# Optimization experiments

Hardware: AMD Instinct MI355X
Metric: run time of the kernel (lower is better)

The kernel has to match this reference:

```python
import jax, jax.numpy as jnp
import numpy as np

K_CONST = 1.0  # margin constant K from __init__


def setup_inputs() -> dict:
    key = jax.random.key(0)
    k1, k2, k3 = jax.random.split(key, 3)
    m, n, d = 2048, 100000, 128
    return {
        "X_tilde": jax.random.normal(k1, (m, d), dtype=jnp.float32),
        "X": jax.random.normal(k2, (n, d), dtype=jnp.float32),
        "w": jax.random.normal(k3, (n, 1), dtype=jnp.float32),
        "k": 10,
    }


def reference(X_tilde, X, w, k):
    # w_prime = sqrt((max(w) - w) / K), appended as extra coordinate for the
    # augmented exact L2 search (queries padded with 0 in that coordinate).
    w_prime2 = (jnp.max(w) - w)[:, 0] / K_CONST  # (n,) == w_prime**2
    # squared L2 in augmented space: ||q||^2 + ||x||^2 + w_prime^2 - 2 q.x
    q2 = jnp.sum(X_tilde * X_tilde, axis=1, keepdims=True)           # (m,1)
    x2 = jnp.sum(X * X, axis=1) + w_prime2                            # (n,)
    d2 = q2 + x2[None, :] - 2.0 * (X_tilde @ X.T)                     # (m,n)
    _, idx = jax.lax.top_k(-d2, k)                                    # (m,k) nearest
    # gather neighbors and recompute actual (non-augmented) L2 distance
    nb = X[idx]                                                       # (m,k,d)
    diff = nb - X_tilde[:, None, :]
    dist = jnp.sqrt(jnp.sum(diff * diff, axis=2))                     # (m,k)
    act = w[idx, 0] - K_CONST * dist                                  # (m,k)
    # argmax + gather == max over the k neighbors
    return jnp.max(act, axis=1)                                       # (m,)
```

## Files before the change

kernel.cpp:

```cpp
#include <hip/hip_runtime.h>
#include <math.h>

typedef __attribute__((ext_vector_type(8))) short short8;
typedef __attribute__((ext_vector_type(16))) float f32x16;

#define D      128
#define NSEG   128
#define SEGC   800
#define NT     25
#define TILE_C 32
#define KTOP   10
#define CAP    128
#define DELTA  3.0f
#define NPAD   (NSEG * SEGC + TILE_C)
#define ROWU   144
#define TUNITS (TILE_C * 18)
#define BUFU   (TUNITS * 8)

__device__ __forceinline__ int lds_unit(int u) {
    int r = u / 18, kb = u % 18;
    return r * 18 + (kb ^ ((r >> 2) & 1));
}

__device__ __forceinline__ ushort f2bf(float f) {
    uint u = __float_as_uint(f);
    uint r = (u + 0x7FFFu + ((u >> 16) & 1u)) >> 16;
    return (ushort)r;
}

__device__ __forceinline__ uint packx2(float x2w) {
    ushort h = f2bf(x2w);
    float hf = __uint_as_float(((uint)h) << 16);
    ushort lo = f2bf(x2w - hf);
    return (uint)h | ((uint)lo << 16);
}

__device__ __forceinline__ void insert10(float s, float v, float ls[KTOP], float lw[KTOP]) {
    ls[9] = s; lw[9] = v;
#pragma unroll
    for (int p = 9; p > 0; --p) {
        bool sw = ls[p] < ls[p - 1];
        float ts = sw ? ls[p - 1] : ls[p];
        float tl = sw ? ls[p]     : ls[p - 1];
        float tv = sw ? lw[p - 1] : lw[p];
        float tu = sw ? lw[p]     : lw[p - 1];
        ls[p] = ts; ls[p - 1] = tl;
        lw[p] = tv; lw[p - 1] = tu;
    }
}

__device__ __forceinline__ void insert10s(float s, float ms[KTOP]) {
    ms[9] = s;
#pragma unroll
    for (int p = 9; p > 0; --p) {
        float a = fminf(ms[p - 1], ms[p]);
        float b = fmaxf(ms[p - 1], ms[p]);
        ms[p - 1] = a; ms[p] = b;
    }
}

__global__ void prep_kernel(const float* __restrict__ Xt, const float* __restrict__ X,
                            const float* __restrict__ w,
                            ushort* __restrict__ Xbp, ushort* __restrict__ Xtb,
                            float* __restrict__ x2wf, float* __restrict__ q2f,
                            int* __restrict__ cnt, int n, int m, int nblocksA) {
    int wave = threadIdx.x >> 6, lane = threadIdx.x & 63;
    if ((int)blockIdx.x < nblocksA) {
        int row = blockIdx.x * 4 + wave;
        if (row >= NPAD) return;
        ushort* rowp = Xbp + (size_t)row * ROWU;
        if (row < n) {
            float2 v = ((const float2*)X)[(size_t)row * 64 + lane];
            ((ushort2*)rowp)[lane] = make_ushort2(f2bf(v.x), f2bf(v.y));
            float s = v.x * v.x + v.y * v.y;
#pragma unroll
            for (int o = 32; o; o >>= 1) s += __shfl_xor(s, o, 64);
            float x2w = s - w[row];
            if (lane == 0) x2wf[row] = x2w;
            if (lane < 8) ((uint*)rowp)[64 + lane] = (lane == 0) ? packx2(x2w) : 0u;
        } else {
            ((ushort2*)rowp)[lane] = make_ushort2(0, 0);
            if (lane < 8) ((uint*)rowp)[64 + lane] = (lane == 0) ? packx2(1e30f) : 0u;
        }
    } else {
        int qb = blockIdx.x - nblocksA;
        int row = qb * 4 + wave;
        int tid = qb * 256 + threadIdx.x;
        if (tid < m) cnt[tid] = 0;
        if (row >= m) return;
        float2 v = ((const float2*)Xt)[(size_t)row * 64 + lane];
        ((ushort2*)Xtb)[(size_t)row * 64 + lane] = make_ushort2(f2bf(v.x), f2bf(v.y));
        float s = v.x * v.x + v.y * v.y;
#pragma unroll
        for (int o = 32; o; o >>= 1) s += __shfl_xor(s, o, 64);
        if (lane == 0) q2f[row] = s;
    }
}

__device__ __forceinline__ void emit_cand(int q, int c, int* cnt, int* buf) {
    int pos = atomicAdd(&cnt[q], 1);
    if (pos < CAP) buf[q * CAP + pos] = c;
}

template<int PASS>
__global__ __launch_bounds__(256, 2) void nd_pass(
        const ushort* __restrict__ Xbp, const ushort* __restrict__ Xtb,
        const float* __restrict__ tau, float* __restrict__ minbuf,
        int* __restrict__ cnt, int* __restrict__ buf, int m) {
    __shared__ __align__(16) ushort As[2 * BUFU];

    const int t = threadIdx.x;
    const int l = t & 63, wv = t >> 6;
    const int half = l >> 5;
    const int seg = blockIdx.x;
    const int qbase = blockIdx.y * 512 + wv * 128;
    const int q0 = qbase + (l & 31);
    const int tile0 = seg * NT;
    const int halfx = half ^ ((l >> 2) & 1);

    short8 Bf[9][4];
#pragma unroll
    for (int s = 0; s < 8; ++s)
#pragma unroll
        for (int qs = 0; qs < 4; ++qs)
            Bf[s][qs] = *(const short8*)(Xtb + (size_t)(q0 + qs * 32) * D + s * 16 + half * 8);
    {
        short8 z = (short8)(short)0;
        if (l < 32) { z[0] = (short)0xBF00; z[1] = (short)0xBF00; }
#pragma unroll
        for (int qs = 0; qs < 4; ++qs) Bf[8][qs] = z;
    }

    float tp[4];
    float mx[4];
#pragma unroll
    for (int qs = 0; qs < 4; ++qs) {
        tp[qs] = (PASS == 2) ? (-0.5f * tau[q0 + qs * 32]) : 0.f;
        mx[qs] = -INFINITY;
    }

    const int u0 = t, u1 = 256 + t, u2 = 512 + (t & 63);
    const int L0 = lds_unit(u0) * 8, L1 = lds_unit(u1) * 8, L2 = lds_unit(u2) * 8;
    const uint4* Xg = (const uint4*)Xbp;

    uint4 r0 = Xg[(size_t)tile0 * TUNITS + u0];
    uint4 r1 = Xg[(size_t)tile0 * TUNITS + u1];
    uint4 r2 = make_uint4(0, 0, 0, 0);
    if (t < 64) r2 = Xg[(size_t)tile0 * TUNITS + u2];

    for (int t2 = 0; t2 < NT; ++t2) {
        ushort* Lb = &As[(t2 & 1) * BUFU];
        *(uint4*)&Lb[L0] = r0;
        *(uint4*)&Lb[L1] = r1;
        if (t < 64) *(uint4*)&Lb[L2] = r2;
        __syncthreads();

        const size_t gb = (size_t)(tile0 + t2 + 1) * TUNITS;
        r0 = Xg[gb + u0];
        r1 = Xg[gb + u1];
        if (t < 64) r2 = Xg[gb + u2];

        f32x16 acc0 = (f32x16)0.f, acc1 = (f32x16)0.f, acc2 = (f32x16)0.f, acc3 = (f32x16)0.f;
#pragma unroll
        for (int ks = 0; ks < 9; ++ks) {
            const int kb = (ks < 8) ? (ks * 2 + halfx) : (16 + halfx);
            short8 a = *(const short8*)&Lb[((l & 31) * 18 + kb) * 8];
            acc0 = __builtin_amdgcn_mfma_f32_32x32x16_bf16(a, Bf[ks][0], acc0, 0, 0, 0);
            acc1 = __builtin_amdgcn_mfma_f32_32x32x16_bf16(a, Bf[ks][1], acc1, 0, 0, 0);
            acc2 = __builtin_amdgcn_mfma_f32_32x32x16_bf16(a, Bf[ks][2], acc2, 0, 0, 0);
            acc3 = __builtin_amdgcn_mfma_f32_32x32x16_bf16(a, Bf[ks][3], acc3, 0, 0, 0);
        }

        float h[4];
#pragma unroll
        for (int qs = 0; qs < 4; ++qs) h[qs] = -INFINITY;
#pragma unroll
        for (int r = 0; r < 16; ++r) {
            h[0] = fmaxf(h[0], acc0[r]); h[1] = fmaxf(h[1], acc1[r]);
            h[2] = fmaxf(h[2], acc2[r]); h[3] = fmaxf(h[3], acc3[r]);
        }
        if (PASS == 1) {
#pragma unroll
            for (int qs = 0; qs < 4; ++qs) mx[qs] = fmaxf(mx[qs], h[qs]);
        } else {
            const int base = (tile0 + t2) * TILE_C;
            if (__any(h[0] >= tp[0])) {
#pragma unroll
                for (int r = 0; r < 16; ++r)
                    if (acc0[r] >= tp[0]) emit_cand(q0,      base + (r & 3) + 8 * (r >> 2) + 4 * half, cnt, buf);
            }
            if (__any(h[1] >= tp[1])) {
#pragma unroll
                for (int r = 0; r < 16; ++r)
                    if (acc1[r] >= tp[1]) emit_cand(q0 + 32, base + (r & 3) + 8 * (r >> 2) + 4 * half, cnt, buf);
            }
            if (__any(h[2] >= tp[2])) {
#pragma unroll
                for (int r = 0; r < 16; ++r)
                    if (acc2[r] >= tp[2]) emit_cand(q0 + 64, base + (r & 3) + 8 * (r >> 2) + 4 * half, cnt, buf);
            }
            if (__any(h[3] >= tp[3])) {
#pragma unroll
                for (int r = 0; r < 16; ++r)
                    if (acc3[r] >= tp[3]) emit_cand(q0 + 96, base + (r & 3) + 8 * (r >> 2) + 4 * half, cnt, buf);
            }
        }
    }

    if (PASS == 1) {
        size_t rowi = (size_t)(seg * 2 + half) * m;
#pragma unroll
        for (int qs = 0; qs < 4; ++qs)
            minbuf[rowi + q0 + qs * 32] = -2.f * mx[qs];
    }
}

__global__ void tau_kernel(const float* __restrict__ minbuf, float* __restrict__ tau, int m) {
    __shared__ float sh[64 * 40];
    const int qi = threadIdx.x & 63, part = threadIdx.x >> 6;
    const int q = blockIdx.x * 64 + qi;
    float ms[KTOP];
#pragma unroll
    for (int e = 0; e < KTOP; ++e) ms[e] = INFINITY;
#pragma unroll 4
    for (int i = 0; i < 64; ++i) {
        float v = minbuf[(size_t)(part * 64 + i) * m + q];
        if (v < ms[9]) insert10s(v, ms);
    }
#pragma unroll
    for (int e = 0; e < KTOP; ++e) sh[qi * 40 + part * 10 + e] = ms[e];
    __syncthreads();
    if (threadIdx.x < 64) {
        const int qq = blockIdx.x * 64 + threadIdx.x;
        float fs[KTOP];
#pragma unroll
        for (int e = 0; e < KTOP; ++e) fs[e] = INFINITY;
        for (int x = 0; x < 40; ++x) {
            float v = sh[threadIdx.x * 40 + x];
            if (v < fs[9]) insert10s(v, fs);
        }
        tau[qq] = fs[9] + DELTA;
    }
}

__global__ void rescore_kernel(const float* __restrict__ Xtf, const float* __restrict__ Xf,
                               const float* __restrict__ w, const float* __restrict__ x2wf,
                               const float* __restrict__ q2f, const int* __restrict__ cnt,
                               const int* __restrict__ buf, float* __restrict__ out, int m) {
    __shared__ float sS[CAP], sW[CAP];
    const int q = blockIdx.x, l = threadIdx.x;
    const int c = min(cnt[q], CAP);
    const bool v0 = l < c, v1 = l + 64 < c;
    const int j0 = v0 ? buf[q * CAP + l] : 0;
    const int j1 = v1 ? buf[q * CAP + l + 64] : 0;
    const float4* Q4 = (const float4*)Xtf + (size_t)q * 32;
    const float4* A4 = (const float4*)Xf + (size_t)j0 * 32;
    const float4* B4 = (const float4*)Xf + (size_t)j1 * 32;
    float acc0 = 0.f, acc1 = 0.f;
#pragma unroll 8
    for (int d = 0; d < 32; ++d) {
        float4 qv = Q4[d];
        float4 a = A4[d], b = B4[d];
        acc0 = fmaf(qv.x, a.x, fmaf(qv.y, a.y, fmaf(qv.z, a.z, fmaf(qv.w, a.w, acc0))));
        acc1 = fmaf(qv.x, b.x, fmaf(qv.y, b.y, fmaf(qv.z, b.z, fmaf(qv.w, b.w, acc1))));
    }
    sS[l]      = v0 ? (x2wf[j0] - 2.f * acc0) : INFINITY;
    sW[l]      = v0 ? w[j0] : 0.f;
    sS[l + 64] = v1 ? (x2wf[j1] - 2.f * acc1) : INFINITY;
    sW[l + 64] = v1 ? w[j1] : 0.f;
    __syncthreads();
    if (l == 0) {
        float ls[KTOP], lw[KTOP];
#pragma unroll
        for (int e = 0; e < KTOP; ++e) { ls[e] = INFINITY; lw[e] = 0.f; }
        for (int i = 0; i < c; ++i)
            if (sS[i] < ls[9]) insert10(sS[i], sW[i], ls, lw);
        float q2v = q2f[q];
        float mxv = -INFINITY;
#pragma unroll
        for (int e = 0; e < KTOP; ++e) {
            if (ls[e] < 1e30f) {
                float d2 = fmaxf(q2v + ls[e] + lw[e], 0.f);
                mxv = fmaxf(mxv, lw[e] - sqrtf(d2));
            }
        }
        out[q] = mxv;
    }
}

extern "C" void kernel_launch(void* const* d_in, const int* in_sizes, int n_in,
                              void* d_out, int out_size, void* d_ws, size_t ws_size,
                              hipStream_t stream) {
    const float* Xt = (const float*)d_in[0];
    const float* X  = (const float*)d_in[1];
    const float* w  = (const float*)d_in[2];
    const int m = in_sizes[0] / D;
    const int n = in_sizes[1] / D;

    auto align256 = [](size_t x) { return (x + 255) & ~(size_t)255; };
    char* p = (char*)d_ws;
    ushort* Xbp  = (ushort*)p;  p += align256((size_t)NPAD * ROWU * 2);
    ushort* Xtb  = (ushort*)p;  p += align256((size_t)m * D * 2);
    float*  x2wf = (float*)p;   p += align256((size_t)n * 4);
    float*  q2f  = (float*)p;   p += align256((size_t)m * 4);
    float*  minb = (float*)p;   p += align256((size_t)2 * NSEG * m * 4);
    float*  tau  = (float*)p;   p += align256((size_t)m * 4);
    int*    cnt  = (int*)p;     p += align256((size_t)m * 4);
    int*    buf  = (int*)p;     p += align256((size_t)m * CAP * 4);

    const int nblocksA = (NPAD + 3) / 4;
    const int nblocksB = (m + 3) / 4;
    prep_kernel<<<nblocksA + nblocksB, 256, 0, stream>>>(Xt, X, w, Xbp, Xtb, x2wf, q2f, cnt, n, m, nblocksA);

    dim3 grid(NSEG, m / 512);
    nd_pass<1><<<grid, 256, 0, stream>>>(Xbp, Xtb, tau, minb, cnt, buf, m);
    tau_kernel<<<m / 64, 256, 0, stream>>>(minb, tau, m);
    nd_pass<2><<<grid, 256, 0, stream>>>(Xbp, Xtb, tau, minb, cnt, buf, m);
    rescore_kernel<<<m, 64, 0, stream>>>(Xt, X, w, x2wf, q2f, cnt, buf, (float*)d_out, m);
}
```

Measured before the change: 269.8 us.

## Load A tiles directly from global into registers, dropping LDS staging

```diff
diff --git a/kernel.cpp b/kernel.cpp
--- a/kernel.cpp
+++ b/kernel.cpp
@@ -15,12 +15,6 @@
 #define NPAD   (NSEG * SEGC + TILE_C)
 #define ROWU   144
 #define TUNITS (TILE_C * 18)
-#define BUFU   (TUNITS * 8)
-
-__device__ __forceinline__ int lds_unit(int u) {
-    int r = u / 18, kb = u % 18;
-    return r * 18 + (kb ^ ((r >> 2) & 1));
-}
 
 __device__ __forceinline__ ushort f2bf(float f) {
     uint u = __float_as_uint(f);
@@ -107,8 +101,6 @@
         const ushort* __restrict__ Xbp, const ushort* __restrict__ Xtb,
         const float* __restrict__ tau, float* __restrict__ minbuf,
         int* __restrict__ cnt, int* __restrict__ buf, int m) {
-    __shared__ __align__(16) ushort As[2 * BUFU];
-
     const int t = threadIdx.x;
     const int l = t & 63, wv = t >> 6;
     const int half = l >> 5;
@@ -116,7 +108,6 @@
     const int qbase = blockIdx.y * 512 + wv * 128;
     const int q0 = qbase + (l & 31);
     const int tile0 = seg * NT;
-    const int halfx = half ^ ((l >> 2) & 1);
 
     short8 Bf[9][4];
 #pragma unroll
@@ -139,37 +130,31 @@
         mx[qs] = -INFINITY;
     }
 
-    const int u0 = t, u1 = 256 + t, u2 = 512 + (t & 63);
-    const int L0 = lds_unit(u0) * 8, L1 = lds_unit(u1) * 8, L2 = lds_unit(u2) * 8;
-    const uint4* Xg = (const uint4*)Xbp;
-
-    uint4 r0 = Xg[(size_t)tile0 * TUNITS + u0];
-    uint4 r1 = Xg[(size_t)tile0 * TUNITS + u1];
-    uint4 r2 = make_uint4(0, 0, 0, 0);
-    if (t < 64) r2 = Xg[(size_t)tile0 * TUNITS + u2];
+    const short8* Xg = (const short8*)Xbp;
+    const int rowu = (l & 31) * 18 + half;
+
+    short8 acur[9], anxt[9];
+    {
+        const size_t gb = (size_t)tile0 * TUNITS + rowu;
+#pragma unroll
+        for (int ks = 0; ks < 9; ++ks)
+            acur[ks] = Xg[gb + ((ks < 8) ? ks * 2 : 16)];
+    }
 
     for (int t2 = 0; t2 < NT; ++t2) {
-        ushort* Lb = &As[(t2 & 1) * BUFU];
-        *(uint4*)&Lb[L0] = r0;
-        *(uint4*)&Lb[L1] = r1;
-        if (t < 64) *(uint4*)&Lb[L2] = r2;
-        __syncthreads();
-
-        const size_t gb = (size_t)(tile0 + t2 + 1) * TUNITS;
-        r0 = Xg[gb + u0];
-        r1 = Xg[gb + u1];
-        if (t < 64) r2 = Xg[gb + u2];
-
+        const size_t gn = (size_t)(tile0 + t2 + 1) * TUNITS + rowu;
         f32x16 acc0 = (f32x16)0.f, acc1 = (f32x16)0.f, acc2 = (f32x16)0.f, acc3 = (f32x16)0.f;
 #pragma unroll
         for (int ks = 0; ks < 9; ++ks) {
-            const int kb = (ks < 8) ? (ks * 2 + halfx) : (16 + halfx);
-            short8 a = *(const short8*)&Lb[((l & 31) * 18 + kb) * 8];
+            anxt[ks] = Xg[gn + ((ks < 8) ? ks * 2 : 16)];
+            short8 a = acur[ks];
             acc0 = __builtin_amdgcn_mfma_f32_32x32x16_bf16(a, Bf[ks][0], acc0, 0, 0, 0);
             acc1 = __builtin_amdgcn_mfma_f32_32x32x16_bf16(a, Bf[ks][1], acc1, 0, 0, 0);
             acc2 = __builtin_amdgcn_mfma_f32_32x32x16_bf16(a, Bf[ks][2], acc2, 0, 0, 0);
             acc3 = __builtin_amdgcn_mfma_f32_32x32x16_bf16(a, Bf[ks][3], acc3, 0, 0, 0);
         }
+#pragma unroll
+        for (int ks = 0; ks < 9; ++ks) acur[ks] = anxt[ks];
 
         float h[4];
 #pragma unroll
@@ -205,6 +190,7 @@
                     if (acc3[r] >= tp[3]) emit_cand(q0 + 96, base + (r & 3) + 8 * (r >> 2) + 4 * half, cnt, buf);
             }
         }
+        __builtin_amdgcn_s_barrier();
     }
 
     if (PASS == 1) {
```

After: 291.3 us. 1.08x slower.
